# Performance work log

Measured on AMD Instinct MI355X. Metric: run time of the kernel, lower is better.

The kernel has to match this reference:

```python
import jax, jax.numpy as jnp
import numpy as np

D_MODEL = 256
D_INNER = 512   # expand * d_model
NHEADS = 8
HEADDIM = 64    # d_inner // nheads
NGROUPS = 1
MDIST = 16


def setup_inputs() -> dict:
    key = jax.random.key(0)
    ks = jax.random.split(key, 12)
    B, L, Q = 4, 2048, 300
    in_key = jax.random.normal(ks[0], (B, L, D_MODEL), jnp.float32)
    in_query = jax.random.normal(ks[1], (B, Q, D_MODEL), jnp.float32)
    dist = jax.random.normal(ks[2], (B, L, Q, MDIST), jnp.float32)

    def lin(k, out_f, in_f):  # torch nn.Linear default init (kaiming-uniform-ish)
        bound = 1.0 / np.sqrt(in_f)
        return jax.random.uniform(k, (out_f, in_f), jnp.float32, -bound, bound)

    W_key = lin(ks[3], 2 * D_INNER + 2 * NGROUPS + NHEADS, D_MODEL)
    W_query = lin(ks[4], D_INNER, D_MODEL)
    W_bc = lin(ks[5], 2 * NGROUPS, MDIST)
    W_dt = lin(ks[6], NHEADS, MDIST)
    # dt_bias init (inverse-softplus of dt sampled log-uniform in [1e-4, 0.1])
    dt_min, dt_max = 1e-4, 0.1
    dtv = jnp.exp(jax.random.uniform(ks[7], (NHEADS,)) * (np.log(dt_max) - np.log(dt_min)) + np.log(dt_min))
    dtv = jnp.clip(dtv, 1e-4, None)
    dt_bias = dtv + jnp.log(-jnp.expm1(-dtv))
    A_log = jnp.log(jax.random.uniform(ks[8], (NHEADS,), minval=1.0, maxval=16.0))
    Dp = jnp.ones((NHEADS,), jnp.float32)
    W_out_key = lin(ks[9], D_MODEL, D_INNER)
    W_out_query = lin(ks[10], D_MODEL, D_INNER)
    key_norm_w = jnp.ones((D_INNER,), jnp.float32)
    ln_w = jnp.ones((D_INNER,), jnp.float32)
    ln_b = jnp.zeros((D_INNER,), jnp.float32)
    return dict(in_key=in_key, in_query=in_query, dist=dist, W_key=W_key, W_query=W_query,
                W_bc=W_bc, W_dt=W_dt, dt_bias=dt_bias, A_log=A_log, Dp=Dp,
                W_out_key=W_out_key, W_out_query=W_out_query, key_norm_w=key_norm_w,
                ln_w=ln_w, ln_b=ln_b)


def _issm_scan(x, S0, dt, A, Bm, Cm, Dp):
    """Selective scan with per-(l,h,n) dt and per-(l,n) B,C (ngroups=1).
    x: (B,L,H,P)  dt: (B,L,H,N)  Bm,Cm: (B,L,N)  S0: (B,H,P,N)  A: (H,)  Dp: (H,)
    """
    xs = (jnp.moveaxis(x, 1, 0), jnp.moveaxis(dt, 1, 0),
          jnp.moveaxis(Bm, 1, 0), jnp.moveaxis(Cm, 1, 0))

    def step(S, inp):
        xl, dtl, Bl, Cl = inp               # (B,H,P), (B,H,N), (B,N), (B,N)
        dA = jnp.exp(dtl * A[None, :, None])            # (B,H,N)
        dBx = (dtl * Bl[:, None, :])[:, :, None, :] * xl[:, :, :, None]
        S = S * dA[:, :, None, :] + dBx                 # (B,H,P,N)
        y = jnp.einsum('bhpn,bn->bhp', S, Cl) + Dp[None, :, None] * xl
        return S, y

    Sf, ys = jax.lax.scan(step, S0, xs)
    return jnp.moveaxis(ys, 0, 1), Sf       # (B,L,H,P), (B,H,P,N)


def reference(in_key, in_query, dist, W_key, W_query, W_bc, W_dt, dt_bias, A_log, Dp,
              W_out_key, W_out_query, key_norm_w, ln_w, ln_b):
    B, L, _ = in_key.shape
    Q = in_query.shape[1]
    zxbcdt = in_key @ W_key.T                            # (B,L,2*Din+2g+H)
    z = zxbcdt[..., :D_INNER]
    x = zxbcdt[..., D_INNER:2 * D_INNER].reshape(B, L, NHEADS, HEADDIM)
    b_bias = zxbcdt[..., 2 * D_INNER:2 * D_INNER + 1]    # (B,L,1)
    c_bias = zxbcdt[..., 2 * D_INNER + 1:2 * D_INNER + 2]
    dt_proj_bias = zxbcdt[..., 2 * D_INNER + 2:]         # (B,L,H)

    # initial state: (B,H,P,Q) -- state dim N == num_queries
    S0 = (in_query @ W_query.T).reshape(B, Q, NHEADS, HEADDIM).transpose(0, 2, 3, 1)
    A = -jnp.exp(A_log)                                  # (H,), constant over state dim

    bc = jnp.einsum('blqm,cm->blqc', dist, W_bc)         # (B,L,Q,2)
    Bm = bc[..., 0] + b_bias                             # (B,L,Q)
    Cm = bc[..., 1] + c_bias
    dtb = jnp.einsum('blqm,hm->blhq', dist, W_dt)        # (B,L,H,Q)
    dt = jax.nn.softplus(dtb + dt_proj_bias[..., None] + dt_bias[None, None, :, None])

    y_f, S_f = _issm_scan(x, S0, dt, A, Bm, Cm, Dp)
    # bidirectional: backward branch uses identical (cloned) x/B/C, flipped along L
    y_b, S_b = _issm_scan(x[:, ::-1], S0, dt[:, ::-1], A, Bm[:, ::-1], Cm[:, ::-1], Dp)
    y = (y_f + y_b[:, ::-1]) * 0.5
    S = (S_f + S_b) * 0.5

    key = y.reshape(B, L, D_INNER)
    g = key * jax.nn.silu(z)                             # gated RMSNorm, norm_before_gate=False
    key = g * jax.lax.rsqrt(jnp.mean(g * g, -1, keepdims=True) + 1e-5) * key_norm_w
    out_key = key @ W_out_key.T

    ls = S.transpose(0, 3, 1, 2).reshape(B, Q, D_INNER)  # b h p q -> b q (h p)
    mu = jnp.mean(ls, -1, keepdims=True)
    var = jnp.mean((ls - mu) ** 2, -1, keepdims=True)
    ls = (ls - mu) * jax.lax.rsqrt(var + 1e-5) * ln_w + ln_b
    out_query = ls @ W_out_query.T
    return out_key, out_query
```

## Files before the change

kernel.cpp:

```cpp
#include <hip/hip_runtime.h>
#include <hip/hip_bf16.h>

#define D_MODEL 256
#define D_INNER 512
#define NHEADS 8
#define HEADDIM 64
#define MDIST 16
#define BB 4
#define LL 2048
#define QQ 300
#define QP 320
#define NSEG 16
#define SEGLEN 128

typedef unsigned short ushort_t;
typedef __attribute__((ext_vector_type(8))) short bf16x8;
typedef __attribute__((ext_vector_type(4))) float f32x4;

__device__ __forceinline__ void bf16_split(float v, ushort_t& hi, ushort_t& lo) {
    __hip_bfloat16 h = __float2bfloat16(v);
    float hf = __bfloat162float(h);
    __hip_bfloat16 l = __float2bfloat16(v - hf);
    hi = *(ushort_t*)&h;
    lo = *(ushort_t*)&l;
}

__global__ __launch_bounds__(256) void c_split(const float* __restrict__ in,
                                               ushort_t* __restrict__ hi,
                                               ushort_t* __restrict__ lo, int n) {
    int i = blockIdx.x * 256 + threadIdx.x;
    if (i >= n) return;
    ushort_t h, l;
    bf16_split(in[i], h, l);
    hi[i] = h;
    lo[i] = l;
}

__global__ __launch_bounds__(256) void gemm_bf16s(const ushort_t* __restrict__ Ah,
                                                  const ushort_t* __restrict__ Al,
                                                  const ushort_t* __restrict__ Bh,
                                                  const ushort_t* __restrict__ Bl,
                                                  float* __restrict__ C,
                                                  int M, int N, int K) {
    int w = threadIdx.x >> 6, lane = threadIdx.x & 63;
    int n0 = blockIdx.x * 64;
    int m0 = blockIdx.y * 128 + w * 32;
    int lm = lane & 15, lk = (lane >> 4) * 8;
    f32x4 acc[2][4];
#pragma unroll
    for (int i = 0; i < 2; i++)
#pragma unroll
        for (int j = 0; j < 4; j++) acc[i][j] = {0.f, 0.f, 0.f, 0.f};

    for (int k0 = 0; k0 < K; k0 += 32) {
        bf16x8 ah[2], al[2], bh[4], blo[4];
#pragma unroll
        for (int mf = 0; mf < 2; mf++) {
            int row = m0 + mf * 16 + lm;
            if (row >= M) row = M - 1;
            size_t off = (size_t)row * K + k0 + lk;
            ah[mf] = *(const bf16x8*)(Ah + off);
            al[mf] = *(const bf16x8*)(Al + off);
        }
#pragma unroll
        for (int nf = 0; nf < 4; nf++) {
            int col = n0 + nf * 16 + lm;
            size_t off = (size_t)col * K + k0 + lk;
            bh[nf]  = *(const bf16x8*)(Bh + off);
            blo[nf] = *(const bf16x8*)(Bl + off);
        }
#pragma unroll
        for (int mf = 0; mf < 2; mf++)
#pragma unroll
            for (int nf = 0; nf < 4; nf++) {
                acc[mf][nf] = __builtin_amdgcn_mfma_f32_16x16x32_bf16(ah[mf], bh[nf],  acc[mf][nf], 0, 0, 0);
                acc[mf][nf] = __builtin_amdgcn_mfma_f32_16x16x32_bf16(ah[mf], blo[nf], acc[mf][nf], 0, 0, 0);
                acc[mf][nf] = __builtin_amdgcn_mfma_f32_16x16x32_bf16(al[mf], bh[nf],  acc[mf][nf], 0, 0, 0);
            }
    }
#pragma unroll
    for (int mf = 0; mf < 2; mf++)
#pragma unroll
        for (int nf = 0; nf < 4; nf++)
#pragma unroll
            for (int r = 0; r < 4; r++) {
                int m = m0 + mf * 16 + (lane >> 4) * 4 + r;
                if (m < M) C[(size_t)m * N + n0 + nf * 16 + lm] = acc[mf][nf][r];
            }
}

__global__ __launch_bounds__(256) void k1b_bias(const float* __restrict__ in_key,
                                                const float* __restrict__ W_key,
                                                float* __restrict__ bias10) {
    int w = threadIdx.x >> 6, lane = threadIdx.x & 63;
    int row = blockIdx.x * 4 + w;
    float4 a = *(const float4*)(in_key + (size_t)row * 256 + lane * 4);
#pragma unroll
    for (int c = 0; c < 10; c++) {
        float4 b = *(const float4*)(W_key + (size_t)(1024 + c) * 256 + lane * 4);
        float t = a.x * b.x + a.y * b.y + a.z * b.z + a.w * b.w;
#pragma unroll
        for (int o = 32; o > 0; o >>= 1) t += __shfl_down(t, o, 64);
        if (lane == 0) bias10[row * 10 + c] = t;
    }
}

__global__ __launch_bounds__(256) void k2_dist(const float* __restrict__ dist,
                                               const float* __restrict__ bias10,
                                               const float* __restrict__ W_bc,
                                               const float* __restrict__ W_dt,
                                               const float* __restrict__ dt_bias,
                                               const float* __restrict__ A_log,
                                               float* __restrict__ dA,
                                               float* __restrict__ dtB,
                                               float* __restrict__ Cm) {
    __shared__ float sWbc[32], sWdt[128], sb[8], sA[8];
    int tid = threadIdx.x;
    if (tid < 32) sWbc[tid] = W_bc[tid];
    else if (tid < 160) sWdt[tid - 32] = W_dt[tid - 32];
    else if (tid < 168) sb[tid - 160] = dt_bias[tid - 160];
    else if (tid < 176) sA[tid - 168] = -expf(A_log[tid - 168]);
    __syncthreads();
    int gid = blockIdx.x * 256 + tid;
    if (gid >= BB * LL * QQ) return;
    int q = gid % QQ;
    int bl = gid / QQ;
    const float* dp = dist + (size_t)gid * 16;
    float d[16];
    float4 d0 = *(const float4*)(dp + 0);
    float4 d1 = *(const float4*)(dp + 4);
    float4 d2 = *(const float4*)(dp + 8);
    float4 d3 = *(const float4*)(dp + 12);
    d[0]=d0.x; d[1]=d0.y; d[2]=d0.z; d[3]=d0.w;
    d[4]=d1.x; d[5]=d1.y; d[6]=d1.z; d[7]=d1.w;
    d[8]=d2.x; d[9]=d2.y; d[10]=d2.z; d[11]=d2.w;
    d[12]=d3.x; d[13]=d3.y; d[14]=d3.z; d[15]=d3.w;
    float bc0 = 0.f, bc1 = 0.f;
#pragma unroll
    for (int m = 0; m < 16; m++) {
        bc0 = fmaf(d[m], sWbc[m], bc0);
        bc1 = fmaf(d[m], sWbc[16 + m], bc1);
    }
    float Bmv = bc0 + bias10[bl * 10 + 0];
    float Cv  = bc1 + bias10[bl * 10 + 1];
    Cm[bl * QP + q] = Cv;
#pragma unroll
    for (int h = 0; h < 8; h++) {
        float t = 0.f;
#pragma unroll
        for (int m = 0; m < 16; m++) t = fmaf(d[m], sWdt[h * 16 + m], t);
        float pre = t + bias10[bl * 10 + 2 + h] + sb[h];
        float dt = (pre > 20.f) ? pre : log1pf(expf(pre));
        int o = (bl * 8 + h) * QP + q;
        dA[o]  = expf(sA[h] * dt);
        dtB[o] = dt * Bmv;
    }
}

__global__ __launch_bounds__(256) void k2b_segdecay(const float* __restrict__ dA,
                                                    float* __restrict__ segd) {
    int gid = blockIdx.x * 256 + threadIdx.x;
    if (gid >= BB * NSEG * 8 * QP) return;
    int q = gid % QP; int r = gid / QP;
    int h = r % 8; r /= 8;
    int s = r % NSEG; int b = r / NSEG;
    int base = ((b * LL + s * SEGLEN) * 8 + h) * QP + q;
    float p = 1.f;
    for (int i = 0; i < SEGLEN; i++) p *= dA[base + i * 8 * QP];
    segd[gid] = p;
}

__global__ __launch_bounds__(512) void pass_ac(const float* __restrict__ dA,
                                               const float* __restrict__ dtB,
                                               const float* __restrict__ Cm,
                                               const float* __restrict__ zx,
                                               float* __restrict__ S_local,
                                               float* __restrict__ yf,
                                               float* __restrict__ yb) {
    __shared__ __align__(16) float sOp[2][2][1024];
    __shared__ float ybuf[2][2][8][64];
    int seg = blockIdx.x, bh = blockIdx.y, dir = blockIdx.z;
    int tid = threadIdx.x;
    int w = tid >> 6, lane = tid & 63;
    int n0 = w * 40;
    int b = bh >> 3, h = bh & 7;
    float S[40];
#pragma unroll
    for (int j = 0; j < 40; j++) S[j] = 0.f;
    float* __restrict__ yo = dir ? yb : yf;

    auto stage = [&](int g, int buf) {
        int it = tid >> 8;
        int pos = (tid & 255) * 4;
        int i = g * 2 + it;
        int l = dir ? (LL - 1 - (seg * SEGLEN + i)) : (seg * SEGLEN + i);
        int bl = b * LL + l;
        const float* src;
        if (pos < 320)      src = dA  + (size_t)(bl * 8 + h) * QP + pos;
        else if (pos < 640) src = dtB + (size_t)(bl * 8 + h) * QP + (pos - 320);
        else if (pos < 960) src = Cm + (size_t)bl * QP + (pos - 640);
        else                src = zx + (size_t)bl * 1024 + 512 + h * 64 + (pos - 960);
        *(float4*)&sOp[buf][it][pos] = *(const float4*)src;
    };
    stage(0, 0);
    const int NG = SEGLEN / 2;
    for (int g = 0; g < NG; g++) {
        __syncthreads();
        if (g + 1 < NG) stage(g + 1, (g + 1) & 1);
        if (g > 0 && tid < 128) {
            int it = tid >> 6, p = tid & 63;
            int i = (g - 1) * 2 + it;
            int l = dir ? (LL - 1 - (seg * SEGLEN + i)) : (seg * SEGLEN + i);
            int bl = b * LL + l;
            const float* yb0 = &ybuf[(g - 1) & 1][it][0][p];
            float t = 0.f;
#pragma unroll
            for (int ww = 0; ww < 8; ww++) t += yb0[ww * 64];
            yo[(size_t)(bl * 8 + h) * 64 + p] = t;
        }
#pragma unroll
        for (int it = 0; it < 2; it++) {
            const float* bufc = sOp[g & 1][it];
            float x = bufc[960 + lane];
            float y = 0.f;
#pragma unroll
            for (int c = 0; c < 10; c++) {
                float4 a4 = *(const float4*)(bufc + n0 + c * 4);
                float4 b4 = *(const float4*)(bufc + 320 + n0 + c * 4);
                float4 c4 = *(const float4*)(bufc + 640 + n0 + c * 4);
                S[c * 4 + 0] = fmaf(S[c * 4 + 0], a4.x, b4.x * x); y = fmaf(S[c * 4 + 0], c4.x, y);
                S[c * 4 + 1] = fmaf(S[c * 4 + 1], a4.y, b4.y * x); y = fmaf(S[c * 4 + 1], c4.y, y);
                S[c * 4 + 2] = fmaf(S[c * 4 + 2], a4.z, b4.z * x); y = fmaf(S[c * 4 + 2], c4.z, y);
                S[c * 4 + 3] = fmaf(S[c * 4 + 3], a4.w, b4.w * x); y = fmaf(S[c * 4 + 3], c4.w, y);
            }
            ybuf[g & 1][it][w][lane] = y;
        }
    }
    __syncthreads();
    if (tid < 128) {
        int it = tid >> 6, p = tid & 63;
        int i = (NG - 1) * 2 + it;
        int l = dir ? (LL - 1 - (seg * SEGLEN + i)) : (seg * SEGLEN + i);
        int bl = b * LL + l;
        const float* yb0 = &ybuf[1][it][0][p];
        float t = 0.f;
#pragma unroll
        for (int ww = 0; ww < 8; ww++) t += yb0[ww * 64];
        yo[(size_t)(bl * 8 + h) * 64 + p] = t;
    }
    size_t base = (size_t)((dir * NSEG + seg) * 32 + bh) * QP * 64;
#pragma unroll
    for (int j = 0; j < 40; j++)
        S_local[base + (size_t)(n0 + j) * 64 + lane] = S[j];
}

__global__ __launch_bounds__(256) void pass_b(const float* __restrict__ S_local,
                                              const float* __restrict__ segd,
                                              const float* __restrict__ S0q,
                                              float* __restrict__ S_in,
                                              float* __restrict__ Savg) {
    int gid = blockIdx.x * 256 + threadIdx.x;
    if (gid >= BB * 8 * QP * 64) return;
    int p = gid & 63; int r = gid >> 6;
    int n = r % QP; r /= QP;
    int h = r & 7; int b = r >> 3;
    int bh = b * 8 + h;
    float s0 = (n < QQ) ? S0q[(size_t)(b * QQ + n) * 512 + h * 64 + p] : 0.f;
    float Sf = 0.f, Sb = 0.f;
    for (int dir = 0; dir < 2; dir++) {
        float S = s0;
        for (int s = 0; s < NSEG; s++) {
            size_t idx = (size_t)(((dir * NSEG + s) * 32 + bh) * QP + n) * 64 + p;
            S_in[idx] = S;
            int sf = dir ? (NSEG - 1 - s) : s;
            float dec = segd[((b * NSEG + sf) * 8 + h) * QP + n];
            S = fmaf(S, dec, S_local[idx]);
        }
        if (dir == 0) Sf = S; else Sb = S;
    }
    Savg[((bh) * QP + n) * 64 + p] = 0.5f * (Sf + Sb);
}

__global__ __launch_bounds__(256) void k3_corr(const float* __restrict__ dA,
                                               const float* __restrict__ Cm,
                                               const float* __restrict__ Sin,
                                               float* __restrict__ yf,
                                               float* __restrict__ yb) {
    __shared__ __align__(16) ushort_t sAh[128][48], sAl[128][48];
    __shared__ __align__(16) ushort_t sBh[64][48], sBl[64][48];
    __shared__ float pref[8][32];
    int seg = blockIdx.x, bh = blockIdx.y, dir = blockIdx.z;
    int b = bh >> 3, h = bh & 7;
    int tid = threadIdx.x;
    int w = tid >> 6, lane = tid & 63;
    int lm = lane & 15, lkq = lane >> 4;
    f32x4 acc[2][4];
#pragma unroll
    for (int i = 0; i < 2; i++)
#pragma unroll
        for (int j = 0; j < 4; j++) acc[i][j] = {0.f, 0.f, 0.f, 0.f};
    size_t sinBase = (size_t)((dir * NSEG + seg) * 32 + bh) * QP * 64;
    int nl = tid & 31, iseg = tid >> 5;

    for (int k0 = 0; k0 < QP; k0 += 32) {
        __syncthreads();
#pragma unroll
        for (int r = 0; r < 8; r++) {
            int flat = tid + r * 256;
            int kn = flat >> 6, p = flat & 63;
            float v = Sin[sinBase + (size_t)(k0 + kn) * 64 + p];
            ushort_t hi, lo;
            bf16_split(v, hi, lo);
            sBh[p][kn] = hi;
            sBl[p][kn] = lo;
        }
        float da[16], cm[16];
#pragma unroll
        for (int k = 0; k < 16; k++) {
            int i = iseg * 16 + k;
            int l = dir ? (LL - 1 - (seg * SEGLEN + i)) : (seg * SEGLEN + i);
            int bl = b * LL + l;
            da[k] = dA[(size_t)(bl * 8 + h) * QP + k0 + nl];
            cm[k] = Cm[(size_t)bl * QP + k0 + nl];
        }
        float lp = 1.f;
#pragma unroll
        for (int k = 0; k < 16; k++) lp *= da[k];
        pref[iseg][nl] = lp;
        __syncthreads();
        if (tid < 32) {
            float c = 1.f;
#pragma unroll
            for (int s = 0; s < 8; s++) {
                float t = pref[s][tid];
                pref[s][tid] = c;
                c *= t;
            }
        }
        __syncthreads();
        float cum = pref[iseg][nl];
#pragma unroll
        for (int k = 0; k < 16; k++) {
            cum *= da[k];
            float v = cum * cm[k];
            ushort_t hi, lo;
            bf16_split(v, hi, lo);
            int i = iseg * 16 + k;
            sAh[i][nl] = hi;
            sAl[i][nl] = lo;
        }
        __syncthreads();
        bf16x8 ah[2], al[2], bhf[4], blf[4];
#pragma unroll
        for (int mf = 0; mf < 2; mf++) {
            int row = w * 32 + mf * 16 + lm;
            ah[mf] = *(const bf16x8*)&sAh[row][lkq * 8];
            al[mf] = *(const bf16x8*)&sAl[row][lkq * 8];
        }
#pragma unroll
        for (int nf = 0; nf < 4; nf++) {
            int p = nf * 16 + lm;
            bhf[nf] = *(const bf16x8*)&sBh[p][lkq * 8];
            blf[nf] = *(const bf16x8*)&sBl[p][lkq * 8];
        }
#pragma unroll
        for (int mf = 0; mf < 2; mf++)
#pragma unroll
            for (int nf = 0; nf < 4; nf++) {
                acc[mf][nf] = __builtin_amdgcn_mfma_f32_16x16x32_bf16(ah[mf], bhf[nf], acc[mf][nf], 0, 0, 0);
                acc[mf][nf] = __builtin_amdgcn_mfma_f32_16x16x32_bf16(ah[mf], blf[nf], acc[mf][nf], 0, 0, 0);
                acc[mf][nf] = __builtin_amdgcn_mfma_f32_16x16x32_bf16(al[mf], bhf[nf], acc[mf][nf], 0, 0, 0);
            }
    }
    float* __restrict__ yo = dir ? yb : yf;
#pragma unroll
    for (int mf = 0; mf < 2; mf++)
#pragma unroll
        for (int nf = 0; nf < 4; nf++)
#pragma unroll
            for (int r = 0; r < 4; r++) {
                int i = w * 32 + mf * 16 + lkq * 4 + r;
                int p = nf * 16 + lm;
                int l = dir ? (LL - 1 - (seg * SEGLEN + i)) : (seg * SEGLEN + i);
                size_t idx = (size_t)((b * LL + l) * 8 + h) * 64 + p;
                yo[idx] += acc[mf][nf][r];
            }
}

__global__ __launch_bounds__(512) void k4_gate(const float* __restrict__ yf,
                                               const float* __restrict__ yb,
                                               const float* __restrict__ zx,
                                               const float* __restrict__ Dp,
                                               const float* __restrict__ knw,
                                               ushort_t* __restrict__ kh,
                                               ushort_t* __restrict__ kl) {
    int bl = blockIdx.x;
    int t = threadIdx.x;
    int h = t >> 6;
    float x = zx[(size_t)bl * 1024 + 512 + t];
    float yv = 0.5f * (yf[(size_t)bl * 512 + t] + yb[(size_t)bl * 512 + t]) + Dp[h] * x;
    float z = zx[(size_t)bl * 1024 + t];
    float g = yv * (z / (1.f + expf(-z)));
    float v = g * g;
#pragma unroll
    for (int o = 32; o > 0; o >>= 1) v += __shfl_down(v, o, 64);
    __shared__ float rs[8];
    __shared__ float stot;
    if ((t & 63) == 0) rs[t >> 6] = v;
    __syncthreads();
    if (t == 0) {
        float s = 0.f;
#pragma unroll
        for (int i = 0; i < 8; i++) s += rs[i];
        stot = s;
    }
    __syncthreads();
    float rms = rsqrtf(stot / 512.f + 1e-5f);
    float kv = g * rms * knw[t];
    ushort_t hi, lo;
    bf16_split(kv, hi, lo);
    kh[(size_t)bl * 512 + t] = hi;
    kl[(size_t)bl * 512 + t] = lo;
}

__global__ __launch_bounds__(512) void k5_ln(const float* __restrict__ Savg,
                                             const float* __restrict__ lnw,
                                             const float* __restrict__ lnb,
                                             ushort_t* __restrict__ lh,
                                             ushort_t* __restrict__ ll) {
    int bq = blockIdx.x;
    int b = bq / QQ, q = bq % QQ;
    int t = threadIdx.x;
    int h = t >> 6, p = t & 63;
    float v = Savg[((b * 8 + h) * QP + q) * 64 + p];
    float s1 = v, s2 = v * v;
#pragma unroll
    for (int o = 32; o > 0; o >>= 1) {
        s1 += __shfl_down(s1, o, 64);
        s2 += __shfl_down(s2, o, 64);
    }
    __shared__ float r1[8], r2[8];
    __shared__ float smu, srv;
    if ((t & 63) == 0) { r1[t >> 6] = s1; r2[t >> 6] = s2; }
    __syncthreads();
    if (t == 0) {
        float a = 0.f, c = 0.f;
#pragma unroll
        for (int i = 0; i < 8; i++) { a += r1[i]; c += r2[i]; }
        float mu = a / 512.f;
        float var = c / 512.f - mu * mu;
        smu = mu;
        srv = rsqrtf(var + 1e-5f);
    }
    __syncthreads();
    float ov = (v - smu) * srv * lnw[t] + lnb[t];
    ushort_t hi, lo;
    bf16_split(ov, hi, lo);
    lh[(size_t)bq * 512 + t] = hi;
    ll[(size_t)bq * 512 + t] = lo;
}

extern "C" void kernel_launch(void* const* d_in, const int* in_sizes, int n_in,
                              void* d_out, int out_size, void* d_ws, size_t ws_size,
                              hipStream_t stream) {
    const float* in_key    = (const float*)d_in[0];
    const float* in_query  = (const float*)d_in[1];
    const float* dist      = (const float*)d_in[2];
    const float* W_key     = (const float*)d_in[3];
    const float* W_query   = (const float*)d_in[4];
    const float* W_bc      = (const float*)d_in[5];
    const float* W_dt      = (const float*)d_in[6];
    const float* dt_bias   = (const float*)d_in[7];
    const float* A_log     = (const float*)d_in[8];
    const float* Dp        = (const float*)d_in[9];
    const float* W_out_key = (const float*)d_in[10];
    const float* W_out_query = (const float*)d_in[11];
    const float* key_norm_w = (const float*)d_in[12];
    const float* ln_w      = (const float*)d_in[13];
    const float* ln_b      = (const float*)d_in[14];

    float* out_key = (float*)d_out;
    float* out_query = out_key + (size_t)BB * LL * D_MODEL;

    char* w8 = (char*)d_ws;
    auto alloc = [&](size_t bytes) {
        char* ptr = w8;
        w8 += (bytes + 255) & ~(size_t)255;
        return ptr;
    };
    float* zx     = (float*)alloc((size_t)8192 * 1024 * 4);
    float* bias10 = (float*)alloc((size_t)8192 * 10 * 4);
    float* S0q    = (float*)alloc((size_t)1200 * 512 * 4);
    float* dAb    = (float*)alloc((size_t)8192 * 8 * QP * 4);
    float* dtBb   = (float*)alloc((size_t)8192 * 8 * QP * 4);
    float* Cmb    = (float*)alloc((size_t)8192 * QP * 4);
    float* segd   = (float*)alloc((size_t)BB * NSEG * 8 * QP * 4);
    float* Sloc   = (float*)alloc((size_t)2 * NSEG * 32 * QP * 64 * 4);
    float* Sin    = (float*)alloc((size_t)2 * NSEG * 32 * QP * 64 * 4);
    float* yfb    = (float*)alloc((size_t)8192 * 512 * 4);
    float* ybb    = (float*)alloc((size_t)8192 * 512 * 4);
    float* Savg   = (float*)alloc((size_t)32 * QP * 64 * 4);
    ushort_t* ink_h  = (ushort_t*)alloc((size_t)2097152 * 2);
    ushort_t* ink_l  = (ushort_t*)alloc((size_t)2097152 * 2);
    ushort_t* wk_h   = (ushort_t*)alloc((size_t)262144 * 2);
    ushort_t* wk_l   = (ushort_t*)alloc((size_t)262144 * 2);
    ushort_t* inq_h  = (ushort_t*)alloc((size_t)307200 * 2);
    ushort_t* inq_l  = (ushort_t*)alloc((size_t)307200 * 2);
    ushort_t* wq_h   = (ushort_t*)alloc((size_t)131072 * 2);
    ushort_t* wq_l   = (ushort_t*)alloc((size_t)131072 * 2);
    ushort_t* keyb_h = (ushort_t*)alloc((size_t)4194304 * 2);
    ushort_t* keyb_l = (ushort_t*)alloc((size_t)4194304 * 2);
    ushort_t* wok_h  = (ushort_t*)alloc((size_t)131072 * 2);
    ushort_t* wok_l  = (ushort_t*)alloc((size_t)131072 * 2);
    ushort_t* lsn_h  = (ushort_t*)alloc((size_t)614400 * 2);
    ushort_t* lsn_l  = (ushort_t*)alloc((size_t)614400 * 2);
    ushort_t* woq_h  = (ushort_t*)alloc((size_t)131072 * 2);
    ushort_t* woq_l  = (ushort_t*)alloc((size_t)131072 * 2);

    c_split<<<8192, 256, 0, stream>>>(in_key, ink_h, ink_l, 2097152);
    c_split<<<1024, 256, 0, stream>>>(W_key, wk_h, wk_l, 262144);
    c_split<<<1200, 256, 0, stream>>>(in_query, inq_h, inq_l, 307200);
    c_split<<<512, 256, 0, stream>>>(W_query, wq_h, wq_l, 131072);
    c_split<<<512, 256, 0, stream>>>(W_out_key, wok_h, wok_l, 131072);
    c_split<<<512, 256, 0, stream>>>(W_out_query, woq_h, woq_l, 131072);

    gemm_bf16s<<<dim3(16, 64), 256, 0, stream>>>(ink_h, ink_l, wk_h, wk_l, zx, 8192, 1024, 256);
    k1b_bias<<<2048, 256, 0, stream>>>(in_key, W_key, bias10);
    gemm_bf16s<<<dim3(8, 10), 256, 0, stream>>>(inq_h, inq_l, wq_h, wq_l, S0q, 1200, 512, 256);

    k2_dist<<<9600, 256, 0, stream>>>(dist, bias10, W_bc, W_dt, dt_bias, A_log, dAb, dtBb, Cmb);
    k2b_segdecay<<<640, 256, 0, stream>>>(dAb, segd);

    pass_ac<<<dim3(NSEG, 32, 2), 512, 0, stream>>>(dAb, dtBb, Cmb, zx, Sloc, yfb, ybb);
    pass_b<<<2560, 256, 0, stream>>>(Sloc, segd, S0q, Sin, Savg);
    k3_corr<<<dim3(NSEG, 32, 2), 256, 0, stream>>>(dAb, Cmb, Sin, yfb, ybb);

    k4_gate<<<8192, 512, 0, stream>>>(yfb, ybb, zx, Dp, key_norm_w, keyb_h, keyb_l);
    gemm_bf16s<<<dim3(4, 64), 256, 0, stream>>>(keyb_h, keyb_l, wok_h, wok_l, out_key, 8192, 256, 512);

    k5_ln<<<1200, 512, 0, stream>>>(Savg, ln_w, ln_b, lsn_h, lsn_l);
    gemm_bf16s<<<dim3(4, 10), 256, 0, stream>>>(lsn_h, lsn_l, woq_h, woq_l, out_query, 1200, 256, 512);
}
```

Measured before the change: 888.8 us.

## Remap scan threads to 4 headdim x 10 state tiles with shuffle reduction

```diff
diff --git a/kernel.cpp b/kernel.cpp
--- a/kernel.cpp
+++ b/kernel.cpp
@@ -183,6 +183,8 @@
     int tid = threadIdx.x;
     int w = tid >> 6, lane = tid & 63;
     int n0 = w * 40;
+    int pgq = lane & 15, ngq = lane >> 4;
+    int nb = n0 + ngq;
     int b = bh >> 3, h = bh & 7;
     float S[40];
 #pragma unroll
@@ -221,19 +223,33 @@
 #pragma unroll
         for (int it = 0; it < 2; it++) {
             const float* bufc = sOp[g & 1][it];
-            float x = bufc[960 + lane];
-            float y = 0.f;
-#pragma unroll
-            for (int c = 0; c < 10; c++) {
-                float4 a4 = *(const float4*)(bufc + n0 + c * 4);
-                float4 b4 = *(const float4*)(bufc + 320 + n0 + c * 4);
-                float4 c4 = *(const float4*)(bufc + 640 + n0 + c * 4);
-                S[c * 4 + 0] = fmaf(S[c * 4 + 0], a4.x, b4.x * x); y = fmaf(S[c * 4 + 0], c4.x, y);
-                S[c * 4 + 1] = fmaf(S[c * 4 + 1], a4.y, b4.y * x); y = fmaf(S[c * 4 + 1], c4.y, y);
-                S[c * 4 + 2] = fmaf(S[c * 4 + 2], a4.z, b4.z * x); y = fmaf(S[c * 4 + 2], c4.z, y);
-                S[c * 4 + 3] = fmaf(S[c * 4 + 3], a4.w, b4.w * x); y = fmaf(S[c * 4 + 3], c4.w, y);
+            float4 xv = *(const float4*)(bufc + 960 + pgq * 4);
+            const float* pa = bufc + nb;
+            float y0 = 0.f, y1 = 0.f, y2 = 0.f, y3 = 0.f;
+#pragma unroll
+            for (int k = 0; k < 10; k++) {
+                float a  = pa[4 * k];
+                float bq = pa[320 + 4 * k];
+                float c  = pa[640 + 4 * k];
+                float s0 = fmaf(S[k * 4 + 0], a, bq * xv.x);
+                float s1 = fmaf(S[k * 4 + 1], a, bq * xv.y);
+                float s2 = fmaf(S[k * 4 + 2], a, bq * xv.z);
+                float s3 = fmaf(S[k * 4 + 3], a, bq * xv.w);
+                S[k * 4 + 0] = s0; y0 = fmaf(s0, c, y0);
+                S[k * 4 + 1] = s1; y1 = fmaf(s1, c, y1);
+                S[k * 4 + 2] = s2; y2 = fmaf(s2, c, y2);
+                S[k * 4 + 3] = s3; y3 = fmaf(s3, c, y3);
             }
-            ybuf[g & 1][it][w][lane] = y;
+            float t0 = __shfl_xor(y0, 16, 64);
+            float t1 = __shfl_xor(y1, 16, 64);
+            float t2 = __shfl_xor(y2, 16, 64);
+            float t3 = __shfl_xor(y3, 16, 64);
+            float z0 = (ngq & 1) ? (y1 + t1) : (y0 + t0);
+            float z1 = (ngq & 1) ? (y3 + t3) : (y2 + t2);
+            float u0 = __shfl_xor(z0, 32, 64);
+            float u1 = __shfl_xor(z1, 32, 64);
+            float yfin = (ngq & 2) ? (z1 + u1) : (z0 + u0);
+            ybuf[g & 1][it][w][pgq * 4 + ngq] = yfin;
         }
     }
     __syncthreads();
@@ -250,8 +266,10 @@
     }
     size_t base = (size_t)((dir * NSEG + seg) * 32 + bh) * QP * 64;
 #pragma unroll
-    for (int j = 0; j < 40; j++)
-        S_local[base + (size_t)(n0 + j) * 64 + lane] = S[j];
+    for (int k = 0; k < 10; k++) {
+        float4 v = {S[k * 4 + 0], S[k * 4 + 1], S[k * 4 + 2], S[k * 4 + 3]};
+        *(float4*)&S_local[base + (size_t)(nb + 4 * k) * 64 + pgq * 4] = v;
+    }
 }
 
 __global__ __launch_bounds__(256) void pass_b(const float* __restrict__ S_local,
```

Result: no change. 884.9 us (-0.4%).

## Remap scan state to lanes-over-N with packed f32x2 FMA and shuffle reductions

Applied to the files above, without the earlier changes.

```diff
diff --git a/kernel.cpp b/kernel.cpp
--- a/kernel.cpp
+++ b/kernel.cpp
@@ -16,6 +16,7 @@
 typedef unsigned short ushort_t;
 typedef __attribute__((ext_vector_type(8))) short bf16x8;
 typedef __attribute__((ext_vector_type(4))) float f32x4;
+typedef __attribute__((ext_vector_type(2))) float f32x2;
 
 __device__ __forceinline__ void bf16_split(float v, ushort_t& hi, ushort_t& lo) {
     __hip_bfloat16 h = __float2bfloat16(v);
@@ -23,6 +24,13 @@
     __hip_bfloat16 l = __float2bfloat16(v - hf);
     hi = *(ushort_t*)&h;
     lo = *(ushort_t*)&l;
+}
+
+__device__ __forceinline__ f32x2 shfl_xor2(f32x2 v, int m) {
+    f32x2 r;
+    r.x = __shfl_xor(v.x, m, 64);
+    r.y = __shfl_xor(v.y, m, 64);
+    return r;
 }
 
 __global__ __launch_bounds__(256) void c_split(const float* __restrict__ in,
@@ -177,81 +185,89 @@
                                                float* __restrict__ S_local,
                                                float* __restrict__ yf,
                                                float* __restrict__ yb) {
-    __shared__ __align__(16) float sOp[2][2][1024];
-    __shared__ float ybuf[2][2][8][64];
+    __shared__ __align__(16) float sOp[2][4096];
     int seg = blockIdx.x, bh = blockIdx.y, dir = blockIdx.z;
     int tid = threadIdx.x;
     int w = tid >> 6, lane = tid & 63;
-    int n0 = w * 40;
     int b = bh >> 3, h = bh & 7;
-    float S[40];
-#pragma unroll
-    for (int j = 0; j < 40; j++) S[j] = 0.f;
+    f32x2 S2[20];
+#pragma unroll
+    for (int j = 0; j < 20; j++) S2[j] = {0.f, 0.f};
     float* __restrict__ yo = dir ? yb : yf;
 
     auto stage = [&](int g, int buf) {
-        int it = tid >> 8;
-        int pos = (tid & 255) * 4;
-        int i = g * 2 + it;
-        int l = dir ? (LL - 1 - (seg * SEGLEN + i)) : (seg * SEGLEN + i);
-        int bl = b * LL + l;
-        const float* src;
-        if (pos < 320)      src = dA  + (size_t)(bl * 8 + h) * QP + pos;
-        else if (pos < 640) src = dtB + (size_t)(bl * 8 + h) * QP + (pos - 320);
-        else if (pos < 960) src = Cm + (size_t)bl * QP + (pos - 640);
-        else                src = zx + (size_t)bl * 1024 + 512 + h * 64 + (pos - 960);
-        *(float4*)&sOp[buf][it][pos] = *(const float4*)src;
+#pragma unroll
+        for (int rep = 0; rep < 2; rep++) {
+            int flat = tid + rep * 512;
+            int it = flat >> 8;
+            int pos = (flat & 255) * 4;
+            int i = g * 4 + it;
+            int l = dir ? (LL - 1 - (seg * SEGLEN + i)) : (seg * SEGLEN + i);
+            int bl = b * LL + l;
+            const float* src;
+            if (pos < 320)      src = dA  + (size_t)(bl * 8 + h) * QP + pos;
+            else if (pos < 640) src = dtB + (size_t)(bl * 8 + h) * QP + (pos - 320);
+            else if (pos < 960) src = Cm + (size_t)bl * QP + (pos - 640);
+            else                src = zx + (size_t)bl * 1024 + 512 + h * 64 + (pos - 960);
+            *(float4*)&sOp[buf][it * 1024 + pos] = *(const float4*)src;
+        }
     };
     stage(0, 0);
-    const int NG = SEGLEN / 2;
-    for (int g = 0; g < NG; g++) {
+    const int NGRP = SEGLEN / 4;
+    for (int g = 0; g < NGRP; g++) {
         __syncthreads();
-        if (g + 1 < NG) stage(g + 1, (g + 1) & 1);
-        if (g > 0 && tid < 128) {
-            int it = tid >> 6, p = tid & 63;
-            int i = (g - 1) * 2 + it;
-            int l = dir ? (LL - 1 - (seg * SEGLEN + i)) : (seg * SEGLEN + i);
-            int bl = b * LL + l;
-            const float* yb0 = &ybuf[(g - 1) & 1][it][0][p];
-            float t = 0.f;
-#pragma unroll
-            for (int ww = 0; ww < 8; ww++) t += yb0[ww * 64];
-            yo[(size_t)(bl * 8 + h) * 64 + p] = t;
-        }
-#pragma unroll
-        for (int it = 0; it < 2; it++) {
-            const float* bufc = sOp[g & 1][it];
-            float x = bufc[960 + lane];
-            float y = 0.f;
-#pragma unroll
-            for (int c = 0; c < 10; c++) {
-                float4 a4 = *(const float4*)(bufc + n0 + c * 4);
-                float4 b4 = *(const float4*)(bufc + 320 + n0 + c * 4);
-                float4 c4 = *(const float4*)(bufc + 640 + n0 + c * 4);
-                S[c * 4 + 0] = fmaf(S[c * 4 + 0], a4.x, b4.x * x); y = fmaf(S[c * 4 + 0], c4.x, y);
-                S[c * 4 + 1] = fmaf(S[c * 4 + 1], a4.y, b4.y * x); y = fmaf(S[c * 4 + 1], c4.y, y);
-                S[c * 4 + 2] = fmaf(S[c * 4 + 2], a4.z, b4.z * x); y = fmaf(S[c * 4 + 2], c4.z, y);
-                S[c * 4 + 3] = fmaf(S[c * 4 + 3], a4.w, b4.w * x); y = fmaf(S[c * 4 + 3], c4.w, y);
-            }
-            ybuf[g & 1][it][w][lane] = y;
-        }
-    }
-    __syncthreads();
-    if (tid < 128) {
-        int it = tid >> 6, p = tid & 63;
-        int i = (NG - 1) * 2 + it;
-        int l = dir ? (LL - 1 - (seg * SEGLEN + i)) : (seg * SEGLEN + i);
-        int bl = b * LL + l;
-        const float* yb0 = &ybuf[1][it][0][p];
-        float t = 0.f;
-#pragma unroll
-        for (int ww = 0; ww < 8; ww++) t += yb0[ww * 64];
-        yo[(size_t)(bl * 8 + h) * 64 + p] = t;
+        if (g + 1 < NGRP) stage(g + 1, (g + 1) & 1);
+        const float* bufg = &sOp[g & 1][0];
+#pragma unroll
+        for (int it = 0; it < 4; it++) {
+            const float* Bq = bufg + it * 1024;
+            float4 xA = *(const float4*)(Bq + 960 + 8 * w);
+            float4 xB = *(const float4*)(Bq + 964 + 8 * w);
+            f32x2 x2[4] = {{xA.x, xA.y}, {xA.z, xA.w}, {xB.x, xB.y}, {xB.z, xB.w}};
+            f32x2 y0 = {0.f, 0.f}, y1 = {0.f, 0.f}, y2v = {0.f, 0.f}, y3 = {0.f, 0.f};
+#pragma unroll
+            for (int k = 0; k < 5; k++) {
+                int idx = k * 64 + lane;
+                float a  = Bq[idx];
+                float bb = Bq[320 + idx];
+                float c  = Bq[640 + idx];
+                f32x2 a2 = {a, a}, b2 = {bb, bb}, c2 = {c, c};
+                f32x2 s;
+                s = S2[k * 4 + 0] * a2 + b2 * x2[0]; S2[k * 4 + 0] = s; y0  += s * c2;
+                s = S2[k * 4 + 1] * a2 + b2 * x2[1]; S2[k * 4 + 1] = s; y1  += s * c2;
+                s = S2[k * 4 + 2] * a2 + b2 * x2[2]; S2[k * 4 + 2] = s; y2v += s * c2;
+                s = S2[k * 4 + 3] * a2 + b2 * x2[3]; S2[k * 4 + 3] = s; y3  += s * c2;
+            }
+            f32x2 g0 = (lane & 1) ? y0 : y1;
+            f32x2 g1 = (lane & 1) ? y2v : y3;
+            g0 = shfl_xor2(g0, 1);
+            g1 = shfl_xor2(g1, 1);
+            f32x2 k0 = ((lane & 1) ? y1 : y0) + g0;
+            f32x2 k1 = ((lane & 1) ? y3 : y2v) + g1;
+            f32x2 gg = (lane & 2) ? k0 : k1;
+            gg = shfl_xor2(gg, 2);
+            f32x2 z = ((lane & 2) ? k1 : k0) + gg;
+            z += shfl_xor2(z, 4);
+            z += shfl_xor2(z, 8);
+            z += shfl_xor2(z, 16);
+            z += shfl_xor2(z, 32);
+            if (lane < 4) {
+                int i = g * 4 + it;
+                int l = dir ? (LL - 1 - (seg * SEGLEN + i)) : (seg * SEGLEN + i);
+                int bl = b * LL + l;
+                *(f32x2*)(yo + (size_t)(bl * 8 + h) * 64 + 8 * w + 2 * lane) = z;
+            }
+        }
     }
     size_t base = (size_t)((dir * NSEG + seg) * 32 + bh) * QP * 64;
 #pragma unroll
-    for (int j = 0; j < 40; j++)
-        S_local[base + (size_t)(n0 + j) * 64 + lane] = S[j];
+    for (int k = 0; k < 5; k++) {
+        int n = k * 64 + lane;
+        float4 v0 = {S2[k * 4 + 0].x, S2[k * 4 + 0].y, S2[k * 4 + 1].x, S2[k * 4 + 1].y};
+        float4 v1 = {S2[k * 4 + 2].x, S2[k * 4 + 2].y, S2[k * 4 + 3].x, S2[k * 4 + 3].y};
+        *(float4*)&S_local[base + (size_t)n * 64 + 8 * w] = v0;
+        *(float4*)&S_local[base + (size_t)n * 64 + 8 * w + 4] = v1;
+    }
 }
 
 __global__ __launch_bounds__(256) void pass_b(const float* __restrict__ S_local,
```

After: 901.3 us. Within noise of the previous version (+1.4%).
